# Kernel tuning notes

Hardware: AMD Instinct MI355X
Metric: run time of the kernel (lower is better)

The kernel has to match this reference:

```python
import jax, jax.numpy as jnp
import numpy as np
import math

B, S, D, H = 2, 2048, 1024, 16
DH = D // H  # dim_per_head = 64


def setup_inputs() -> dict:
    key = jax.random.key(0)
    ks = jax.random.split(key, 12)
    s = 1.0 / math.sqrt(D)
    return {
        "key": jax.random.normal(ks[0], (B, S, D), jnp.float32),
        "value": jax.random.normal(ks[1], (B, S, D), jnp.float32),
        "query": jax.random.normal(ks[2], (B, S, D), jnp.float32),
        "mask": jax.random.randint(ks[3], (B, S, S), 0, 2).astype(bool),
        "Wq": jax.random.normal(ks[4], (D, D), jnp.float32) * s,
        "bq": jnp.zeros((D,), jnp.float32),
        "Wk": jax.random.normal(ks[5], (D, D), jnp.float32) * s,
        "bk": jnp.zeros((D,), jnp.float32),
        "Wv": jax.random.normal(ks[6], (D, D), jnp.float32) * s,
        "bv": jnp.zeros((D,), jnp.float32),
        "Wo": jax.random.normal(ks[7], (D, D), jnp.float32) * s,
        "bo": jnp.zeros((D,), jnp.float32),
    }


def _shape(x):
    # [B, S, D] -> [B, H, S, DH]
    return x.reshape(B, -1, H, DH).transpose(0, 2, 1, 3)


def reference(key, value, query, mask, Wq, bq, Wk, bk, Wv, bv, Wo, bo):
    q = _shape(query @ Wq.T + bq)  # [B,H,Sq,DH]
    k = _shape(key @ Wk.T + bk)    # [B,H,Sk,DH]
    v = _shape(value @ Wv.T + bv)  # [B,H,Sk,DH]
    q = q / jnp.sqrt(jnp.asarray(DH, q.dtype))
    scores = jnp.einsum("bhqd,bhkd->bhqk", q, k)
    scores = jnp.where(mask[:, None, :, :], jnp.asarray(-1e18, scores.dtype), scores)
    attn = jax.nn.softmax(scores, axis=-1)
    # dropout is identity in eval/deterministic reference
    ctx = jnp.einsum("bhqk,bhkd->bhqd", attn, v)
    ctx = ctx.transpose(0, 2, 1, 3).reshape(B, -1, D)  # unshape
    return ctx @ Wo.T + bo
```

## Files before the change

### kernel.cpp

```cpp
#include <hip/hip_runtime.h>
#include <math.h>


constexpr int Bc  = 2;
constexpr int Sc  = 2048;
constexpr int Dc  = 1024;
constexpr int Hc  = 16;
constexpr int DHc = 64;
constexpr int BSc = Bc * Sc;

constexpr float LOG2E = 1.4426950408889634f;

typedef __bf16 bf16x8 __attribute__((ext_vector_type(8)));
typedef __bf16 bf16x4 __attribute__((ext_vector_type(4)));
typedef float  f32x4  __attribute__((ext_vector_type(4)));

#define GLDS16(gp, lp) __builtin_amdgcn_global_load_lds( \
    (const __attribute__((address_space(1))) void*)(gp), \
    (__attribute__((address_space(3))) void*)(lp), 16, 0, 0)

__global__ __launch_bounds__(256)
void wsplit(const float* __restrict__ W0, const float* __restrict__ W1,
            const float* __restrict__ W2, const float* __restrict__ W3,
            __bf16* __restrict__ out)
{
    const float* src[4] = {W0, W1, W2, W3};
    const int z = blockIdx.y;
    const size_t idx = ((size_t)blockIdx.x * 256 + threadIdx.x) * 4;
    const float4 v = *(const float4*)&src[z][idx];
    bf16x4 o;
    o[0] = (__bf16)v.x; o[1] = (__bf16)v.y; o[2] = (__bf16)v.z; o[3] = (__bf16)v.w;
    *(bf16x4*)&out[(size_t)z * Dc * Dc + idx] = o;
}

__device__ __forceinline__ void sweep128s(const float* __restrict__ A,
                                          const __bf16* __restrict__ Wh,
                                          __bf16* As, __bf16* Ws,
                                          int gm0, int gn0, f32x4 acc[4][4])
{
    const int tid  = threadIdx.x;
    const int w    = tid >> 6;
    const int lane = tid & 63;
    const int cc   = lane & 15;
    const int g    = lane >> 4;
    const int wm   = (w & 1) * 64;
    const int wn   = (w >> 1) * 64;

    for (int k0 = 0; k0 < Dc; k0 += 64) {
        __syncthreads();
#pragma unroll
        for (int r = 0; r < 4; ++r) {
            const int L  = r * 256 + tid;
            const int wr = L >> 3;
            const int sl = L & 7;
            const int c  = sl ^ (wr & 7);
            GLDS16(Wh + (size_t)(gn0 + wr) * Dc + k0 + c * 8,
                   (char*)Ws + (r * 256 + w * 64) * 16);
        }
#pragma unroll
        for (int i = 0; i < 8; ++i) {
            const int Lq = i * 256 + tid;
            const int ar = Lq >> 4;
            const int aq = Lq & 15;
            const float4 v = *(const float4*)&A[(size_t)(gm0 + ar) * Dc + k0 + aq * 4];
            const int off = ar * 128 +
                        ((((aq >> 1) ^ (ar & 7)) << 4) | ((aq & 1) << 3));
            bf16x4 hv;
            hv[0] = (__bf16)v.x; hv[1] = (__bf16)v.y;
            hv[2] = (__bf16)v.z; hv[3] = (__bf16)v.w;
            *(bf16x4*)((char*)As + off) = hv;
        }
        __syncthreads();
#pragma unroll
        for (int kk = 0; kk < 2; ++kk) {
            const int cb4 = (kk * 4 + g) << 4;
            bf16x8 af[4], bfr[4];
#pragma unroll
            for (int mt = 0; mt < 4; ++mt) {
                const int row = wm + mt * 16 + cc;
                af[mt] = *(const bf16x8*)((const char*)As + row * 128 +
                                          (cb4 ^ ((row & 7) << 4)));
            }
#pragma unroll
            for (int nt = 0; nt < 4; ++nt) {
                const int row = wn + nt * 16 + cc;
                bfr[nt] = *(const bf16x8*)((const char*)Ws + row * 128 +
                                           (cb4 ^ ((row & 7) << 4)));
            }
#pragma unroll
            for (int mt = 0; mt < 4; ++mt)
#pragma unroll
                for (int nt = 0; nt < 4; ++nt)
                    acc[mt][nt] = __builtin_amdgcn_mfma_f32_16x16x32_bf16(
                        af[mt], bfr[nt], acc[mt][nt], 0, 0, 0);
        }
    }
}

__device__ __forceinline__ void sweep64b(const __bf16* __restrict__ Ahi,
                                         const __bf16* __restrict__ Alo,
                                         const __bf16* __restrict__ Wh,
                                         __bf16* AsHi, __bf16* AsLo, __bf16* Ws,
                                         int gm0, int gn0, f32x4 acc[2][4])
{
    const int tid  = threadIdx.x;
    const int w    = tid >> 6;
    const int lane = tid & 63;
    const int cc   = lane & 15;
    const int g    = lane >> 4;
    const int wm   = (w & 1) * 32;
    const int wn   = (w >> 1) * 64;

    for (int k0 = 0; k0 < Dc; k0 += 64) {
        __syncthreads();
#pragma unroll
        for (int r = 0; r < 4; ++r) {
            const int L  = r * 256 + tid;
            const int wr = L >> 3;
            const int sl = L & 7;
            const int c  = sl ^ (wr & 7);
            GLDS16(Wh + (size_t)(gn0 + wr) * Dc + k0 + c * 8,
                   (char*)Ws + (r * 256 + w * 64) * 16);
        }
#pragma unroll
        for (int r = 0; r < 2; ++r) {
            const int L  = r * 256 + tid;
            const int wr = L >> 3;
            const int sl = L & 7;
            const int c  = sl ^ (wr & 7);
            GLDS16(Ahi + (size_t)(gm0 + wr) * Dc + k0 + c * 8,
                   (char*)AsHi + (r * 256 + w * 64) * 16);
            GLDS16(Alo + (size_t)(gm0 + wr) * Dc + k0 + c * 8,
                   (char*)AsLo + (r * 256 + w * 64) * 16);
        }
        __syncthreads();
#pragma unroll
        for (int kk = 0; kk < 2; ++kk) {
            const int cb4 = (kk * 4 + g) << 4;
            bf16x8 ahi[2], alo[2], bfr[4];
#pragma unroll
            for (int mt = 0; mt < 2; ++mt) {
                const int row = wm + mt * 16 + cc;
                const int off = row * 128 + (cb4 ^ ((row & 7) << 4));
                ahi[mt] = *(const bf16x8*)((const char*)AsHi + off);
                alo[mt] = *(const bf16x8*)((const char*)AsLo + off);
            }
#pragma unroll
            for (int nt = 0; nt < 4; ++nt) {
                const int row = wn + nt * 16 + cc;
                bfr[nt] = *(const bf16x8*)((const char*)Ws + row * 128 +
                                           (cb4 ^ ((row & 7) << 4)));
            }
#pragma unroll
            for (int mt = 0; mt < 2; ++mt)
#pragma unroll
                for (int nt = 0; nt < 4; ++nt) {
                    acc[mt][nt] = __builtin_amdgcn_mfma_f32_16x16x32_bf16(
                        ahi[mt], bfr[nt], acc[mt][nt], 0, 0, 0);
                    acc[mt][nt] = __builtin_amdgcn_mfma_f32_16x16x32_bf16(
                        alo[mt], bfr[nt], acc[mt][nt], 0, 0, 0);
                }
        }
    }
}

__global__ __launch_bounds__(256)
void qkv_mfma(const float* __restrict__ query, const float* __restrict__ key,
              const float* __restrict__ value, const __bf16* __restrict__ Whi,
              const float* __restrict__ bq, const float* __restrict__ bk,
              const float* __restrict__ bv,
              __bf16* __restrict__ Qo, __bf16* __restrict__ Ko, __bf16* __restrict__ Vt)
{
    __shared__ __align__(16) __bf16 As[8192];
    __shared__ __align__(16) __bf16 Ws[8192];

    const int z = blockIdx.z;
    const float* A    = (z == 0) ? query : (z == 1) ? key : value;
    const float* bias = (z == 0) ? bq    : (z == 1) ? bk  : bv;
    const float scale = (z == 0) ? 0.125f * LOG2E : 1.0f;
    const __bf16* Wh  = Whi + (size_t)z * Dc * Dc;

    const int gm0 = blockIdx.x * 128;
    const int gn0 = blockIdx.y * 128;

    f32x4 acc[4][4];
#pragma unroll
    for (int mt = 0; mt < 4; ++mt)
#pragma unroll
        for (int nt = 0; nt < 4; ++nt) acc[mt][nt] = {0.f, 0.f, 0.f, 0.f};

    sweep128s(A, Wh, As, Ws, gm0, gn0, acc);

    const int tid = threadIdx.x;
    const int w = tid >> 6, lane = tid & 63;
    const int cc = lane & 15, g = lane >> 4;
    const int wm = (w & 1) * 64, wn = (w >> 1) * 64;

    float bias4[4];
#pragma unroll
    for (int nt = 0; nt < 4; ++nt) bias4[nt] = bias[gn0 + wn + nt * 16 + cc];

    if (z == 2) {
#pragma unroll
        for (int mt = 0; mt < 4; ++mt)
#pragma unroll
            for (int nt = 0; nt < 4; ++nt) {
                const int col = gn0 + wn + nt * 16 + cc;
                const int h = col >> 6, dh = col & 63;
                const int row0 = gm0 + wm + mt * 16 + g * 4;
                const int b = row0 >> 11, s0 = row0 & 2047;
                bf16x4 vv;
#pragma unroll
                for (int reg = 0; reg < 4; ++reg)
                    vv[reg] = (__bf16)(acc[mt][nt][reg] + bias4[nt]);
                *(bf16x4*)&Vt[(((size_t)(b * Hc + h)) * DHc + dh) * Sc + s0] = vv;
            }
    } else {
        __bf16* O = (z == 0) ? Qo : Ko;
#pragma unroll
        for (int mt = 0; mt < 4; ++mt)
#pragma unroll
            for (int nt = 0; nt < 4; ++nt) {
                const int col = gn0 + wn + nt * 16 + cc;
                const int h = col >> 6, dh = col & 63;
#pragma unroll
                for (int reg = 0; reg < 4; ++reg) {
                    const int row = gm0 + wm + mt * 16 + g * 4 + reg;
                    const int b = row >> 11, s = row & 2047;
                    O[(((size_t)(b * Hc + h)) * Sc + s) * DHc + dh] =
                        (__bf16)((acc[mt][nt][reg] + bias4[nt]) * scale);
                }
            }
    }
}

__global__ __launch_bounds__(256)
void out_mfma(const __bf16* __restrict__ ctxHi, const __bf16* __restrict__ ctxLo,
              const __bf16* __restrict__ Wohi,
              const float* __restrict__ bo, float* __restrict__ out)
{
    __shared__ __align__(16) __bf16 AsHi[4096];
    __shared__ __align__(16) __bf16 AsLo[4096];
    __shared__ __align__(16) __bf16 Ws[8192];

    const int gm0 = blockIdx.x * 64;
    const int gn0 = blockIdx.y * 128;

    f32x4 acc[2][4];
#pragma unroll
    for (int mt = 0; mt < 2; ++mt)
#pragma unroll
        for (int nt = 0; nt < 4; ++nt) acc[mt][nt] = {0.f, 0.f, 0.f, 0.f};

    sweep64b(ctxHi, ctxLo, Wohi, AsHi, AsLo, Ws, gm0, gn0, acc);

    const int tid = threadIdx.x;
    const int w = tid >> 6, lane = tid & 63;
    const int cc = lane & 15, g = lane >> 4;
    const int wm = (w & 1) * 32, wn = (w >> 1) * 64;

    float bias4[4];
#pragma unroll
    for (int nt = 0; nt < 4; ++nt) bias4[nt] = bo[gn0 + wn + nt * 16 + cc];

#pragma unroll
    for (int mt = 0; mt < 2; ++mt)
#pragma unroll
        for (int nt = 0; nt < 4; ++nt) {
            const int col = gn0 + wn + nt * 16 + cc;
#pragma unroll
            for (int reg = 0; reg < 4; ++reg) {
                const int row = gm0 + wm + mt * 16 + g * 4 + reg;
                out[(size_t)row * Dc + col] = acc[mt][nt][reg] + bias4[nt];
            }
        }
}

__global__ __launch_bounds__(256)
void mask_pack(const int* __restrict__ mask, unsigned long long* __restrict__ out)
{
    const int lane = threadIdx.x & 63;
    const size_t waveBase = ((size_t)blockIdx.x * 4 + (threadIdx.x >> 6)) * 256;
    unsigned long long b0 = __ballot(mask[waveBase + lane]        != 0);
    unsigned long long b1 = __ballot(mask[waveBase + 64 + lane]   != 0);
    unsigned long long b2 = __ballot(mask[waveBase + 128 + lane]  != 0);
    unsigned long long b3 = __ballot(mask[waveBase + 192 + lane]  != 0);
    if (lane == 0) {
        unsigned long long* dst = out + (waveBase >> 6);
        dst[0] = b0; dst[1] = b1; dst[2] = b2; dst[3] = b3;
    }
}

__global__ __launch_bounds__(512, 2)
void attn_mfma(const __bf16* __restrict__ Q, const __bf16* __restrict__ K,
               const __bf16* __restrict__ Vt,
               const unsigned long long* __restrict__ mp,
               __bf16* __restrict__ ctxHi, __bf16* __restrict__ ctxLo)
{
    __shared__ __align__(16) char smem[49152];

    const int tid  = threadIdx.x;
    const int w    = tid >> 6;
    const int lane = tid & 63;
    const int cc   = lane & 15;
    const int g    = lane >> 4;
    const int qg   = w & 3;
    const int kh   = w >> 2;
    const int bh   = blockIdx.y;
    const int b    = bh >> 4;
    const int h    = bh & 15;
    const int qw   = blockIdx.x * 128 + qg * 32;

    const __bf16* Qb  = Q  + (size_t)bh * Sc * DHc;
    const __bf16* Kb  = K  + (size_t)bh * Sc * DHc;
    const __bf16* Vtb = Vt + (size_t)bh * DHc * Sc;

    char* Ks = smem + kh * 16384;
    char* Vs = smem + kh * 16384 + 8192;
    char* Pw = smem + 32768 + w * 2048;

    bf16x8 qa[2][2];
#pragma unroll
    for (int mt = 0; mt < 2; ++mt) {
        qa[mt][0] = *(const bf16x8*)&Qb[(size_t)(qw + mt * 16 + cc) * DHc + g * 8];
        qa[mt][1] = *(const bf16x8*)&Qb[(size_t)(qw + mt * 16 + cc) * DHc + 32 + g * 8];
    }

    f32x4 o[2][4] = {};
    float l[2][4] = {};

    const int t4 = tid & 255;
    const int sr = t4 >> 3;
    const int sl = t4 & 7;
    const int ck = sl ^ (sr & 7);
    const int kbase = kh * (Sc / 2);

    bf16x8 pk0 = *(const bf16x8*)&Kb[(size_t)(kbase + sr) * DHc + ck * 8];
    bf16x8 pk1 = *(const bf16x8*)&Kb[(size_t)(kbase + sr + 32) * DHc + ck * 8];
    bf16x8 pv0 = *(const bf16x8*)&Vtb[(size_t)sr * Sc + kbase + ck * 8];
    bf16x8 pv1 = *(const bf16x8*)&Vtb[(size_t)(sr + 32) * Sc + kbase + ck * 8];

    for (int it = 0; it < 16; ++it) {
        const int k0 = kbase + it * 64;
        __syncthreads();
        *(bf16x8*)(Ks + sr * 128 + sl * 16)        = pk0;
        *(bf16x8*)(Ks + (sr + 32) * 128 + sl * 16) = pk1;
        *(bf16x8*)(Vs + sr * 128 + sl * 16)        = pv0;
        *(bf16x8*)(Vs + (sr + 32) * 128 + sl * 16) = pv1;
        __syncthreads();

        if (it < 15) {
            const int kn = k0 + 64;
            pk0 = *(const bf16x8*)&Kb[(size_t)(kn + sr) * DHc + ck * 8];
            pk1 = *(const bf16x8*)&Kb[(size_t)(kn + sr + 32) * DHc + ck * 8];
            pv0 = *(const bf16x8*)&Vtb[(size_t)sr * Sc + kn + ck * 8];
            pv1 = *(const bf16x8*)&Vtb[(size_t)(sr + 32) * Sc + kn + ck * 8];
        }

        unsigned long long mw[2][4];
#pragma unroll
        for (int mt = 0; mt < 2; ++mt)
#pragma unroll
            for (int r = 0; r < 4; ++r)
                mw[mt][r] = mp[(size_t)(b * Sc + qw + mt * 16 + g * 4 + r) * (Sc / 64)
                               + (k0 >> 6)];

        f32x4 sc[2][4];
#pragma unroll
        for (int nt = 0; nt < 4; ++nt) {
            const int row = nt * 16 + cc;
            const int rx  = (row & 7) << 4;
            const bf16x8 kb0 = *(const bf16x8*)(Ks + row * 128 + ((g << 4) ^ rx));
            const bf16x8 kb1 = *(const bf16x8*)(Ks + row * 128 + ((64 + (g << 4)) ^ rx));
            f32x4 z0 = {-24.f, -24.f, -24.f, -24.f};
            z0 = __builtin_amdgcn_mfma_f32_16x16x32_bf16(qa[0][0], kb0, z0, 0, 0, 0);
            z0 = __builtin_amdgcn_mfma_f32_16x16x32_bf16(qa[0][1], kb1, z0, 0, 0, 0);
            sc[0][nt] = z0;
            f32x4 z1 = {-24.f, -24.f, -24.f, -24.f};
            z1 = __builtin_amdgcn_mfma_f32_16x16x32_bf16(qa[1][0], kb0, z1, 0, 0, 0);
            z1 = __builtin_amdgcn_mfma_f32_16x16x32_bf16(qa[1][1], kb1, z1, 0, 0, 0);
            sc[1][nt] = z1;
        }

        bf16x8 pa[2][2];
#pragma unroll
        for (int mt = 0; mt < 2; ++mt) {
            unsigned mlo[4], mhi[4];
#pragma unroll
            for (int r = 0; r < 4; ++r) {
                const unsigned long long sh = mw[mt][r] >> cc;
                mlo[r] = (unsigned)sh;
                mhi[r] = (unsigned)(sh >> 32);
            }
#pragma unroll
            for (int nt = 0; nt < 4; ++nt)
#pragma unroll
                for (int r = 0; r < 4; ++r) {
                    float p = __builtin_amdgcn_exp2f(sc[mt][nt][r]);
                    const unsigned bit =
                        (nt == 0) ? (mlo[r] & 1u) :
                        (nt == 1) ? (mlo[r] & 0x10000u) :
                        (nt == 2) ? (mhi[r] & 1u) : (mhi[r] & 0x10000u);
                    p = bit ? 0.f : p;
                    l[mt][r] += p;
                    *(__bf16*)(Pw + (g * 4 + r) * 128 +
                               (((nt ^ g) << 5) | (cc << 1))) = (__bf16)p;
                }
            const int sw = (cc >> 2) << 5;
            pa[mt][0] = *(const bf16x8*)(Pw + cc * 128 + ((g * 16) ^ sw));
            pa[mt][1] = *(const bf16x8*)(Pw + cc * 128 + ((64 + g * 16) ^ sw));
        }

#pragma unroll
        for (int nt = 0; nt < 4; ++nt) {
            const int row = nt * 16 + cc;
            const int rx  = (row & 7) << 4;
            const bf16x8 vb0 = *(const bf16x8*)(Vs + row * 128 + ((g << 4) ^ rx));
            const bf16x8 vb1 = *(const bf16x8*)(Vs + row * 128 + ((64 + (g << 4)) ^ rx));
            o[0][nt] = __builtin_amdgcn_mfma_f32_16x16x32_bf16(pa[0][0], vb0, o[0][nt], 0, 0, 0);
            o[0][nt] = __builtin_amdgcn_mfma_f32_16x16x32_bf16(pa[0][1], vb1, o[0][nt], 0, 0, 0);
            o[1][nt] = __builtin_amdgcn_mfma_f32_16x16x32_bf16(pa[1][0], vb0, o[1][nt], 0, 0, 0);
            o[1][nt] = __builtin_amdgcn_mfma_f32_16x16x32_bf16(pa[1][1], vb1, o[1][nt], 0, 0, 0);
        }
    }

#pragma unroll
    for (int off = 1; off < 16; off <<= 1)
#pragma unroll
        for (int mt = 0; mt < 2; ++mt)
#pragma unroll
            for (int r = 0; r < 4; ++r)
                l[mt][r] += __shfl_xor(l[mt][r], off, 16);

    __syncthreads();
    float* Oc = (float*)(smem + 16384);
    float* Lc = (float*)smem;
    if (kh) {
#pragma unroll
        for (int mt = 0; mt < 2; ++mt) {
#pragma unroll
            for (int nt = 0; nt < 4; ++nt)
#pragma unroll
                for (int r = 0; r < 4; ++r)
                    Oc[(qg * 32 + mt * 16 + g * 4 + r) * 64 + nt * 16 + cc] =
                        o[mt][nt][r];
            if (cc == 0)
#pragma unroll
                for (int r = 0; r < 4; ++r)
                    Lc[qg * 32 + mt * 16 + g * 4 + r] = l[mt][r];
        }
    }
    __syncthreads();
    if (!kh) {
#pragma unroll
        for (int mt = 0; mt < 2; ++mt)
#pragma unroll
            for (int r = 0; r < 4; ++r) {
                const int row = qg * 32 + mt * 16 + g * 4 + r;
                const float lt = l[mt][r] + Lc[row];
                const float inv = 1.0f / lt;
                const int q = blockIdx.x * 128 + row;
#pragma unroll
                for (int nt = 0; nt < 4; ++nt) {
                    const size_t idx =
                        ((size_t)b * Sc + q) * Dc + h * 64 + nt * 16 + cc;
                    const float v = (o[mt][nt][r] + Oc[row * 64 + nt * 16 + cc]) * inv;
                    const __bf16 hi = (__bf16)v;
                    ctxHi[idx] = hi;
                    ctxLo[idx] = (__bf16)(v - (float)hi);
                }
            }
    }
}

extern "C" void kernel_launch(void* const* d_in, const int* in_sizes, int n_in,
                              void* d_out, int out_size, void* d_ws, size_t ws_size,
                              hipStream_t stream)
{
    const float* key   = (const float*)d_in[0];
    const float* value = (const float*)d_in[1];
    const float* query = (const float*)d_in[2];
    const int*   mask  = (const int*)  d_in[3];
    const float* Wq    = (const float*)d_in[4];
    const float* bq    = (const float*)d_in[5];
    const float* Wk    = (const float*)d_in[6];
    const float* bk    = (const float*)d_in[7];
    const float* Wv    = (const float*)d_in[8];
    const float* bv    = (const float*)d_in[9];
    const float* Wo    = (const float*)d_in[10];
    const float* bo    = (const float*)d_in[11];
    float* out = (float*)d_out;

    char* wsb = (char*)d_ws;
    __bf16* Qbf  = (__bf16*)(wsb);
    __bf16* Kbf  = (__bf16*)(wsb + ((size_t)8  << 20));
    __bf16* Vt   = (__bf16*)(wsb + ((size_t)16 << 20));
    unsigned long long* mpk = (unsigned long long*)(wsb + ((size_t)32 << 20));
    __bf16* Whi  = (__bf16*)(wsb + ((size_t)33 << 20));
    __bf16* ctxHi = (__bf16*)(wsb + ((size_t)41 << 20));
    __bf16* ctxLo = (__bf16*)(wsb + ((size_t)49 << 20));

    dim3 gws(Dc * Dc / (256 * 4), 4);
    wsplit<<<gws, 256, 0, stream>>>(Wq, Wk, Wv, Wo, Whi);

    dim3 gqkv(BSc / 128, Dc / 128, 3);
    qkv_mfma<<<gqkv, 256, 0, stream>>>(query, key, value, Whi, bq, bk, bv,
                                       Qbf, Kbf, Vt);

    const int mask_n = Bc * Sc * Sc;
    mask_pack<<<mask_n / 1024, 256, 0, stream>>>(mask, mpk);

    dim3 gattn(Sc / 128, Bc * Hc);
    attn_mfma<<<gattn, 512, 0, stream>>>(Qbf, Kbf, Vt, mpk, ctxHi, ctxLo);

    dim3 gout(BSc / 64, Dc / 128);
    out_mfma<<<gout, 256, 0, stream>>>(ctxHi, ctxLo, Whi + (size_t)3 * Dc * Dc,
                                       bo, out);
}
```

Measured before the change: 304.8 us.

## Drop key-split in attention, double-buffer K/V tiles via async global-to-LDS loads

Attention blocks shrink from 512 to 256 threads. Each wave now covers the full key range for its 32 query rows instead of splitting keys across two wave groups, so the LDS-based merge of partial outputs and row sums at the end is removed. K and V tiles are double-buffered in shared memory and filled with global_load_lds direct copies issued one tile ahead, replacing the register-staged prefetch and one of the two barriers per iteration. The trade-off is half as many waves per block and twice as many loop iterations per wave, which may cut latency hiding. Correctness also relies on the async LDS loads being complete before the barrier that precedes their use.

```diff
diff --git a/kernel.cpp b/kernel.cpp
--- a/kernel.cpp
+++ b/kernel.cpp
@@ -291,32 +291,28 @@
     }
 }
 
-__global__ __launch_bounds__(512, 2)
+__global__ __launch_bounds__(256, 2)
 void attn_mfma(const __bf16* __restrict__ Q, const __bf16* __restrict__ K,
                const __bf16* __restrict__ Vt,
                const unsigned long long* __restrict__ mp,
                __bf16* __restrict__ ctxHi, __bf16* __restrict__ ctxLo)
 {
-    __shared__ __align__(16) char smem[49152];
+    __shared__ __align__(16) char smem[40960];
 
     const int tid  = threadIdx.x;
     const int w    = tid >> 6;
     const int lane = tid & 63;
     const int cc   = lane & 15;
     const int g    = lane >> 4;
-    const int qg   = w & 3;
-    const int kh   = w >> 2;
     const int bh   = blockIdx.y;
     const int b    = bh >> 4;
     const int h    = bh & 15;
-    const int qw   = blockIdx.x * 128 + qg * 32;
+    const int qw   = blockIdx.x * 128 + w * 32;
 
     const __bf16* Qb  = Q  + (size_t)bh * Sc * DHc;
     const __bf16* Kb  = K  + (size_t)bh * Sc * DHc;
     const __bf16* Vtb = Vt + (size_t)bh * DHc * Sc;
 
-    char* Ks = smem + kh * 16384;
-    char* Vs = smem + kh * 16384 + 8192;
     char* Pw = smem + 32768 + w * 2048;
 
     bf16x8 qa[2][2];
@@ -329,32 +325,40 @@
     f32x4 o[2][4] = {};
     float l[2][4] = {};
 
-    const int t4 = tid & 255;
-    const int sr = t4 >> 3;
-    const int sl = t4 & 7;
-    const int ck = sl ^ (sr & 7);
-    const int kbase = kh * (Sc / 2);
-
-    bf16x8 pk0 = *(const bf16x8*)&Kb[(size_t)(kbase + sr) * DHc + ck * 8];
-    bf16x8 pk1 = *(const bf16x8*)&Kb[(size_t)(kbase + sr + 32) * DHc + ck * 8];
-    bf16x8 pv0 = *(const bf16x8*)&Vtb[(size_t)sr * Sc + kbase + ck * 8];
-    bf16x8 pv1 = *(const bf16x8*)&Vtb[(size_t)(sr + 32) * Sc + kbase + ck * 8];
-
-    for (int it = 0; it < 16; ++it) {
-        const int k0 = kbase + it * 64;
+    const int ci[2] = {tid, 256 + tid};
+    int  rowi[2], ski[2];
+#pragma unroll
+    for (int i = 0; i < 2; ++i) {
+        rowi[i] = ci[i] >> 3;
+        const int sl = ci[i] & 7;
+        ski[i] = sl ^ (rowi[i] & 7);
+    }
+
+#pragma unroll
+    for (int i = 0; i < 2; ++i) {
+        GLDS16(Kb + (size_t)rowi[i] * DHc + ski[i] * 8,
+               smem + ci[i] * 16);
+        GLDS16(Vtb + (size_t)rowi[i] * Sc + ski[i] * 8,
+               smem + 8192 + ci[i] * 16);
+    }
+
+    for (int it = 0; it < 32; ++it) {
+        const int k0 = it * 64;
+        char* Ks = smem + (it & 1) * 16384;
+        char* Vs = Ks + 8192;
+
         __syncthreads();
-        *(bf16x8*)(Ks + sr * 128 + sl * 16)        = pk0;
-        *(bf16x8*)(Ks + (sr + 32) * 128 + sl * 16) = pk1;
-        *(bf16x8*)(Vs + sr * 128 + sl * 16)        = pv0;
-        *(bf16x8*)(Vs + (sr + 32) * 128 + sl * 16) = pv1;
-        __syncthreads();
-
-        if (it < 15) {
+
+        if (it + 1 < 32) {
+            char* Kn = smem + ((it + 1) & 1) * 16384;
             const int kn = k0 + 64;
-            pk0 = *(const bf16x8*)&Kb[(size_t)(kn + sr) * DHc + ck * 8];
-            pk1 = *(const bf16x8*)&Kb[(size_t)(kn + sr + 32) * DHc + ck * 8];
-            pv0 = *(const bf16x8*)&Vtb[(size_t)sr * Sc + kn + ck * 8];
-            pv1 = *(const bf16x8*)&Vtb[(size_t)(sr + 32) * Sc + kn + ck * 8];
+#pragma unroll
+            for (int i = 0; i < 2; ++i) {
+                GLDS16(Kb + (size_t)(kn + rowi[i]) * DHc + ski[i] * 8,
+                       Kn + ci[i] * 16);
+                GLDS16(Vtb + (size_t)rowi[i] * Sc + kn + ski[i] * 8,
+                       Kn + 8192 + ci[i] * 16);
+            }
         }
 
         unsigned long long mw[2][4];
@@ -432,45 +436,21 @@
             for (int r = 0; r < 4; ++r)
                 l[mt][r] += __shfl_xor(l[mt][r], off, 16);
 
-    __syncthreads();
-    float* Oc = (float*)(smem + 16384);
-    float* Lc = (float*)smem;
-    if (kh) {
-#pragma unroll
-        for (int mt = 0; mt < 2; ++mt) {
-#pragma unroll
-            for (int nt = 0; nt < 4; ++nt)
-#pragma unroll
-                for (int r = 0; r < 4; ++r)
-                    Oc[(qg * 32 + mt * 16 + g * 4 + r) * 64 + nt * 16 + cc] =
-                        o[mt][nt][r];
-            if (cc == 0)
-#pragma unroll
-                for (int r = 0; r < 4; ++r)
-                    Lc[qg * 32 + mt * 16 + g * 4 + r] = l[mt][r];
-        }
-    }
-    __syncthreads();
-    if (!kh) {
-#pragma unroll
-        for (int mt = 0; mt < 2; ++mt)
-#pragma unroll
-            for (int r = 0; r < 4; ++r) {
-                const int row = qg * 32 + mt * 16 + g * 4 + r;
-                const float lt = l[mt][r] + Lc[row];
-                const float inv = 1.0f / lt;
-                const int q = blockIdx.x * 128 + row;
-#pragma unroll
-                for (int nt = 0; nt < 4; ++nt) {
-                    const size_t idx =
-                        ((size_t)b * Sc + q) * Dc + h * 64 + nt * 16 + cc;
-                    const float v = (o[mt][nt][r] + Oc[row * 64 + nt * 16 + cc]) * inv;
-                    const __bf16 hi = (__bf16)v;
-                    ctxHi[idx] = hi;
-                    ctxLo[idx] = (__bf16)(v - (float)hi);
-                }
-            }
-    }
+#pragma unroll
+    for (int mt = 0; mt < 2; ++mt)
+#pragma unroll
+        for (int r = 0; r < 4; ++r) {
+            const float inv = 1.0f / l[mt][r];
+            const int q = qw + mt * 16 + g * 4 + r;
+#pragma unroll
+            for (int nt = 0; nt < 4; ++nt) {
+                const size_t idx = ((size_t)b * Sc + q) * Dc + h * 64 + nt * 16 + cc;
+                const float v = o[mt][nt][r] * inv;
+                const __bf16 hi = (__bf16)v;
+                ctxHi[idx] = hi;
+                ctxLo[idx] = (__bf16)(v - (float)hi);
+            }
+        }
 }
 
 extern "C" void kernel_launch(void* const* d_in, const int* in_sizes, int n_in,
@@ -511,7 +491,7 @@
     mask_pack<<<mask_n / 1024, 256, 0, stream>>>(mask, mpk);
 
     dim3 gattn(Sc / 128, Bc * Hc);
-    attn_mfma<<<gattn, 512, 0, stream>>>(Qbf, Kbf, Vt, mpk, ctxHi, ctxLo);
+    attn_mfma<<<gattn, 256, 0, stream>>>(Qbf, Kbf, Vt, mpk, ctxHi, ctxLo);
 
     dim3 gout(BSc / 64, Dc / 128);
     out_mfma<<<gout, 256, 0, stream>>>(ctxHi, ctxLo, Whi + (size_t)3 * Dc * Dc,
```

Measured after the change: 287.6 us. 5.6% less time.
